# Optimization experiments

Measured on AMD Instinct MI355X. Metric: run time of the kernel, lower is better.

Reference implementation:

```python
import jax, jax.numpy as jnp
import numpy as np

B, C, H, W = 4, 288, 64, 64
P = 2
HEADS = 36
MLP_RATIO = 4.0
D = C * P * P              # hidden_size = 1152
HF = int(D * MLP_RATIO)    # 4608
LN_EPS = 1e-6
ATTN_EPS = 1e-8


def _layernorm(x):
    # LayerNorm over [C,H,W] per sample, no affine
    mu = jnp.mean(x, axis=(1, 2, 3), keepdims=True)
    var = jnp.mean((x - mu) ** 2, axis=(1, 2, 3), keepdims=True)
    return (x - mu) * jax.lax.rsqrt(var + LN_EPS)


def _seg(x):
    # b c (n1 p) (n2 p) -> b (n1 n2) (c p p)
    b, c, h, w = x.shape
    n1, n2 = h // P, w // P
    x = x.reshape(b, c, n1, P, n2, P).transpose(0, 2, 4, 1, 3, 5)
    return x.reshape(b, n1 * n2, c * P * P)


def _comb(t, h, w):
    # b (n1 n2) (c p p) -> b c (n1 p) (n2 p)
    b, n, dd = t.shape
    n1, n2 = h // P, w // P
    c = dd // (P * P)
    x = t.reshape(b, n1, n2, c, P, P).transpose(0, 3, 1, 4, 2, 5)
    return x.reshape(b, c, h, w)


def _lite_la(t, qkv_w, proj_w, proj_b):
    # ReLU-kernel linear attention with ones-padding normalization trick
    b, s, dm = t.shape
    d = dm // HEADS
    qkv = t @ qkv_w.T                       # [b,s,3*dm]
    q, k, v = jnp.split(qkv, 3, axis=-1)
    q = jax.nn.relu(q).reshape(b, s, HEADS, d)
    k = jax.nn.relu(k).reshape(b, s, HEADS, d)
    v = v.reshape(b, s, HEADS, d)
    v = jnp.concatenate([v, jnp.ones((b, s, HEADS, 1), v.dtype)], axis=-1)  # PAD_VAL=1
    vk = jnp.einsum('bshe,bshd->bhed', v, k)       # [b,h,d+1,d]
    out = jnp.einsum('bhed,bshd->bshe', vk, q)     # [b,s,h,d+1]
    out = out[..., :-1] / (out[..., -1:] + ATTN_EPS)
    return out.reshape(b, s, dm) @ proj_w.T + proj_b


def _glumb(t, inv_w, inv_b, dw_w, dw_b, pw_w):
    # GLU MBConv: 1x1 expand + SiLU -> 3x3 depthwise -> GLU gate -> 1x1 project
    b, n, c = t.shape
    hp = wp = int(n ** 0.5)
    x = t.reshape(b, hp, wp, c).transpose(0, 3, 1, 2)  # NCHW
    x = jnp.einsum('bchw,oc->bohw', x, inv_w[:, :, 0, 0]) + inv_b[None, :, None, None]
    x = jax.nn.silu(x)
    x = jax.lax.conv_general_dilated(x, dw_w, (1, 1), 'SAME',
                                     feature_group_count=dw_w.shape[0],
                                     dimension_numbers=('NCHW', 'OIHW', 'NCHW'))
    x = x + dw_b[None, :, None, None]
    x, gate = jnp.split(x, 2, axis=1)
    x = x * jax.nn.silu(gate)
    x = jnp.einsum('bchw,oc->bohw', x, pw_w[:, :, 0, 0])
    return x.reshape(b, c, n).transpose(0, 2, 1)


def setup_inputs() -> dict:
    key = jax.random.key(0)
    ks = jax.random.split(key, 10)
    s = 0.02
    return {
        'x': jax.random.normal(ks[0], (B, C, H, W), jnp.float32),
        'cond': jax.random.normal(ks[1], (B, 6 * C, H, W), jnp.float32),
        'global_token': jax.random.normal(ks[2], (B, D), jnp.float32),
        'time_token': jax.random.normal(ks[3], (B, D), jnp.float32),
        'ss_w': jax.random.normal(ks[4], (6 * C, 6 * C, 1, 1), jnp.float32) * s,
        'ss_b': jnp.zeros((6 * C,), jnp.float32),
        'qkv_w': jax.random.normal(ks[5], (3 * D, D), jnp.float32) * s,
        'proj_w': jax.random.normal(ks[6], (D, D), jnp.float32) * s,
        'proj_b': jnp.zeros((D,), jnp.float32),
        'inv_w': jax.random.normal(ks[7], (2 * HF, D, 1, 1), jnp.float32) * s,
        'inv_b': jnp.zeros((2 * HF,), jnp.float32),
        'dw_w': jax.random.normal(ks[8], (2 * HF, 1, 3, 3), jnp.float32) * s,
        'dw_b': jnp.zeros((2 * HF,), jnp.float32),
        'pw_w': jax.random.normal(ks[9], (D, HF, 1, 1), jnp.float32) * s,
    }


def reference(x, cond, global_token, time_token, ss_w, ss_b, qkv_w, proj_w, proj_b,
              inv_w, inv_b, dw_w, dw_b, pw_w):
    # scale_shift_table: SiLU + 1x1 conv on cond, chunk into 6 per-channel maps
    ss = jnp.einsum('bchw,oc->bohw', jax.nn.silu(cond), ss_w[:, :, 0, 0]) + ss_b[None, :, None, None]
    sh_msa, sc_msa, g_msa, sh_mlp, sc_mlp, g_mlp = jnp.split(ss, 6, axis=1)
    # attention branch
    tok = _seg(_layernorm(x) * (1.0 + sc_msa) + sh_msa)
    tok = jnp.concatenate([global_token[:, None], time_token[:, None], tok], axis=1)
    a = _lite_la(tok, qkv_w, proj_w, proj_b)
    x = x + _comb(a[:, 2:], H, W) * g_msa
    # MLP branch
    m = _glumb(_seg(_layernorm(x) * (1.0 + sc_mlp) + sh_mlp), inv_w, inv_b, dw_w, dw_b, pw_w)
    x = x + _comb(m, H, W) * g_mlp
    return x
```

## Files before the change

kernel.cpp:

```cpp
#include <hip/hip_runtime.h>
#include <hip/hip_bf16.h>
#include <cstdint>


typedef __bf16 bf16;
typedef bf16 bf16x8 __attribute__((ext_vector_type(8)));
typedef bf16 bf16x4 __attribute__((ext_vector_type(4)));
typedef float f32x4 __attribute__((ext_vector_type(4)));

typedef const __attribute__((address_space(1))) void gas_void;
typedef __attribute__((address_space(3))) void las_void;

__device__ __forceinline__ void gload16(const bf16* g, bf16* l) {
    __builtin_amdgcn_global_load_lds((gas_void*)g, (las_void*)l, 16, 0, 0);
}

#define BB 4
#define CC 288
#define HW 4096
#define C6 1728
#define DD 1152
#define SEQ 1026
#define RTOT 4104
#define NTOK 1024
#define HF 4608
#define HF2 9216
#define NPB 1179648

static constexpr size_t OFF_SUMS = 0;
static constexpr size_t OFF_SS   = 256;
static constexpr size_t SS_BYTES = (size_t)C6 * 16384 * 2;
static constexpr size_t OFF_R2   = OFF_SS + SS_BYTES;
static constexpr size_t OFF_PART1= OFF_R2;
static constexpr size_t OFF_A1   = OFF_R2;
static constexpr size_t OFF_T    = OFF_R2;
static constexpr size_t OFF_QKV  = OFF_T   + (size_t)RTOT*DD*2;
static constexpr size_t OFF_PART2= OFF_QKV;
static constexpr size_t OFF_VK   = OFF_QKV + (size_t)3456*RTOT*2;
static constexpr size_t OFF_ATT  = OFF_VK  + (size_t)144*1056*4;
static constexpr size_t OFF_APROJ= OFF_ATT + (size_t)RTOT*DD*2;
static constexpr size_t OFF_T2   = OFF_R2;
static constexpr size_t OFF_Y    = OFF_T2  + (size_t)4096*DD*2;
static constexpr size_t OFF_G    = OFF_Y   + (size_t)4096*HF2*2;
static constexpr size_t OFF_M    = OFF_G   + (size_t)4096*HF*2;
static constexpr size_t OFF_W    = OFF_R2  + 132120576;
static constexpr size_t OFF_WSS  = OFF_W;
static constexpr size_t OFF_WQKV = OFF_WSS  + (size_t)C6*C6*2;
static constexpr size_t OFF_WPROJ= OFF_WQKV + (size_t)3456*DD*2;
static constexpr size_t OFF_WINV = OFF_WPROJ+ (size_t)DD*DD*2;
static constexpr size_t OFF_WPW  = OFF_WINV + (size_t)HF2*DD*2;

__global__ __launch_bounds__(256) void cvt_bf16(const float* __restrict__ s,
                                                bf16* __restrict__ d, int n4) {
    int i = blockIdx.x * 256 + threadIdx.x;
    if (i < n4) {
        float4 v = ((const float4*)s)[i];
        bf16x4 o = {(bf16)v.x, (bf16)v.y, (bf16)v.z, (bf16)v.w};
        ((bf16x4*)d)[i] = o;
    }
}

__device__ __forceinline__ void block_reduce2_store(float s1, float s2, float* dst) {
    #pragma unroll
    for (int o = 32; o > 0; o >>= 1) { s1 += __shfl_down(s1, o); s2 += __shfl_down(s2, o); }
    __shared__ float r1[4], r2[4];
    int wave = threadIdx.x >> 6, lane = threadIdx.x & 63;
    if (lane == 0) { r1[wave] = s1; r2[wave] = s2; }
    __syncthreads();
    if (threadIdx.x == 0) {
        dst[0] = r1[0] + r1[1] + r1[2] + r1[3];
        dst[1] = r2[0] + r2[1] + r2[2] + r2[3];
    }
}

__global__ __launch_bounds__(256) void ln_stats(const float* __restrict__ x, float* __restrict__ part) {
    const float* base = x + (size_t)blockIdx.x * 4096;
    float s1 = 0.f, s2 = 0.f;
    #pragma unroll
    for (int it = 0; it < 4; it++) {
        float4 v = ((const float4*)base)[it * 256 + threadIdx.x];
        s1 += v.x + v.y + v.z + v.w;
        s2 += v.x * v.x + v.y * v.y + v.z * v.z + v.w * v.w;
    }
    block_reduce2_store(s1, s2, part + (size_t)blockIdx.x * 2);
}

__global__ __launch_bounds__(256) void reduce_part(const float* __restrict__ part, float* __restrict__ sums,
                                                   int nper, int out_off) {
    int b = blockIdx.x;
    float s1 = 0.f, s2 = 0.f;
    for (int i = threadIdx.x; i < nper; i += 256) {
        s1 += part[(size_t)(b * nper + i) * 2];
        s2 += part[(size_t)(b * nper + i) * 2 + 1];
    }
    block_reduce2_store(s1, s2, sums + out_off + b * 2);
}

__global__ __launch_bounds__(256) void prep_cond(const float* __restrict__ cond, bf16* __restrict__ A1) {
    __shared__ float tile[64][65];
    int b = blockIdx.z, k0 = blockIdx.y * 64, h0 = blockIdx.x * 64;
    int col = threadIdx.x & 63, r4 = threadIdx.x >> 6;
    const float* src = cond + ((size_t)b * C6 + k0) * HW + h0;
    #pragma unroll
    for (int p = 0; p < 16; p++) {
        int kk = r4 + p * 4;
        float v = src[(size_t)kk * HW + col];
        tile[col][kk] = v / (1.f + __expf(-v));
    }
    __syncthreads();
    bf16* dst = A1 + ((size_t)(b * HW + h0)) * C6 + k0;
    #pragma unroll
    for (int p = 0; p < 16; p++) {
        int rr = r4 + p * 4;
        dst[(size_t)rr * C6 + col] = (bf16)tile[rr][col];
    }
}

template <int EP, int BIAS>
__global__ __launch_bounds__(256) void gemm_bt(const bf16* __restrict__ A, const bf16* __restrict__ B,
                                               const float* __restrict__ bias, bf16* __restrict__ C,
                                               int M, int N, int K, int reluLimit) {
    __shared__ __align__(16) bf16 As[128 * 32];
    __shared__ __align__(16) bf16 Bs[128 * 32];
    const int tid = threadIdx.x, wave = tid >> 6, lane = tid & 63;
    const int m0 = blockIdx.y * 128, n0 = blockIdx.x * 128;

    const int c0 = wave * 128 + lane;
    const int c1 = c0 + 64;
    const int sw = ((c0 >> 2) & 3) ^ ((c0 >> 4) & 3);
    const int ka = (((c0 & 3) ^ sw)) * 8;
    int ra0 = min(m0 + (c0 >> 2), M - 1), ra1 = min(m0 + (c1 >> 2), M - 1);
    int rb0 = min(n0 + (c0 >> 2), N - 1), rb1 = min(n0 + (c1 >> 2), N - 1);
    const bf16* gA0 = A + (size_t)ra0 * K + ka;
    const bf16* gA1 = A + (size_t)ra1 * K + ka;
    const bf16* gB0 = B + (size_t)rb0 * K + ka;
    const bf16* gB1 = B + (size_t)rb1 * K + ka;
    bf16* lA0 = As + wave * 1024;
    bf16* lA1 = As + wave * 1024 + 512;
    bf16* lB0 = Bs + wave * 1024;
    bf16* lB1 = Bs + wave * 1024 + 512;

    const int wm = (wave >> 1) * 64, wn = (wave & 1) * 64;
    const int l15 = lane & 15;
    const int sr = (l15 & 3) ^ ((l15 >> 2) & 3);
    const int fc = ((lane >> 4) ^ sr) * 8;
    const bf16* fa = As + (wm + l15) * 32 + fc;
    const bf16* fb = Bs + (wn + l15) * 32 + fc;

    f32x4 acc[4][4];
    #pragma unroll
    for (int i = 0; i < 4; i++)
        #pragma unroll
        for (int j = 0; j < 4; j++) acc[i][j] = (f32x4){0.f, 0.f, 0.f, 0.f};

    for (int kt = 0; kt < K; kt += 32) {
        __syncthreads();
        gload16(gA0, lA0); gload16(gA1, lA1);
        gload16(gB0, lB0); gload16(gB1, lB1);
        gA0 += 32; gA1 += 32; gB0 += 32; gB1 += 32;
        __syncthreads();
        bf16x8 af[4], bv[4];
        #pragma unroll
        for (int i = 0; i < 4; i++) af[i] = *(const bf16x8*)(fa + i * 16 * 32);
        #pragma unroll
        for (int j = 0; j < 4; j++) bv[j] = *(const bf16x8*)(fb + j * 16 * 32);
        #pragma unroll
        for (int i = 0; i < 4; i++)
            #pragma unroll
            for (int j = 0; j < 4; j++)
                acc[i][j] = __builtin_amdgcn_mfma_f32_16x16x32_bf16(af[i], bv[j], acc[i][j], 0, 0, 0);
    }

    const int mq = (lane >> 4) * 4, nl = lane & 15;
    #pragma unroll
    for (int i = 0; i < 4; i++) {
        #pragma unroll
        for (int j = 0; j < 4; j++) {
            int n = n0 + wn + j * 16 + nl;
            if (n < N) {
                #pragma unroll
                for (int r = 0; r < 4; r++) {
                    int m = m0 + wm + i * 16 + mq + r;
                    if (m < M) {
                        float v = acc[i][j][r];
                        if (BIAS == 1) v += bias[m];
                        else if (BIAS == 2) v += bias[n];
                        if (EP == 1) { if (m < reluLimit) v = fmaxf(v, 0.f); }
                        else if (EP == 2) { v = v / (1.f + __expf(-v)); }
                        C[(size_t)m * N + n] = (bf16)v;
                    }
                }
            }
        }
    }
}

__global__ __launch_bounds__(256) void build_tok(const float* __restrict__ x, const float* __restrict__ gtok,
                                                 const float* __restrict__ ttok, const bf16* __restrict__ ss,
                                                 const float* __restrict__ sums, bf16* __restrict__ T) {
    int row = blockIdx.x;
    int b = row / SEQ, s = row % SEQ;
    bf16* dst = T + (size_t)row * DD;
    if (s == 0) {
        for (int d = threadIdx.x; d < DD; d += 256) dst[d] = (bf16)gtok[b * DD + d];
        return;
    }
    if (s == 1) {
        for (int d = threadIdx.x; d < DD; d += 256) dst[d] = (bf16)ttok[b * DD + d];
        return;
    }
    float mu = sums[b * 2] * (1.f / (float)NPB);
    float var = sums[b * 2 + 1] * (1.f / (float)NPB) - mu * mu;
    float rsig = rsqrtf(var + 1e-6f);
    int n = s - 2, n1 = n >> 5, n2 = n & 31;
    for (int dd = threadIdx.x; dd < DD; dd += 256) {
        int c = dd >> 2, p1 = (dd >> 1) & 1, p2 = dd & 1;
        int hw = (n1 * 2 + p1) * 64 + n2 * 2 + p2;
        float xv = x[((size_t)b * CC + c) * HW + hw];
        float sc = (float)ss[(size_t)(288 + c) * 16384 + b * HW + hw];
        float sh = (float)ss[(size_t)(0 + c) * 16384 + b * HW + hw];
        dst[dd] = (bf16)((xv - mu) * rsig * (1.f + sc) + sh);
    }
}

__global__ __launch_bounds__(256) void attn_vk(const bf16* __restrict__ qkv, float* __restrict__ vk) {
    int bh = blockIdx.x >> 2, sb = blockIdx.x & 3;
    int b = bh / 36, h = bh % 36;
    int s_begin = sb * 288;
    int s_end = min(s_begin + 288, SEQ);
    const bf16* kbase = qkv + (size_t)(DD + h * 32) * RTOT + b * SEQ;
    const bf16* vbase = qkv + (size_t)(2 * DD + h * 32) * RTOT + b * SEQ;
    __shared__ __align__(16) bf16 kk[32][80];
    __shared__ __align__(16) bf16 vv[32][80];
    int tid = threadIdx.x;
    int e = tid >> 3, dg = (tid & 7) * 4;
    int lrow = tid >> 3, lcol = (tid & 7) * 8;
    float a0 = 0.f, a1 = 0.f, a2 = 0.f, a3 = 0.f, aD = 0.f;
    for (int s0 = s_begin; s0 < s_end; s0 += 64) {
        __syncthreads();
        #pragma unroll
        for (int j = 0; j < 8; j++) {
            int s = s0 + lcol + j;
            bool ok = s < s_end;
            kk[lrow][lcol + j] = ok ? kbase[(size_t)lrow * RTOT + s] : (bf16)0.f;
            vv[lrow][lcol + j] = ok ? vbase[(size_t)lrow * RTOT + s] : (bf16)0.f;
        }
        __syncthreads();
        #pragma unroll
        for (int j0 = 0; j0 < 64; j0 += 8) {
            bf16x8 vvv = *(const bf16x8*)&vv[e][j0];
            bf16x8 k0 = *(const bf16x8*)&kk[dg + 0][j0];
            bf16x8 k1 = *(const bf16x8*)&kk[dg + 1][j0];
            bf16x8 k2 = *(const bf16x8*)&kk[dg + 2][j0];
            bf16x8 k3 = *(const bf16x8*)&kk[dg + 3][j0];
            #pragma unroll
            for (int j = 0; j < 8; j++) {
                float vf = (float)vvv[j];
                a0 += vf * (float)k0[j];
                a1 += vf * (float)k1[j];
                a2 += vf * (float)k2[j];
                a3 += vf * (float)k3[j];
            }
            if (tid < 32) {
                bf16x8 kd = *(const bf16x8*)&kk[tid][j0];
                #pragma unroll
                for (int j = 0; j < 8; j++) aD += (float)kd[j];
            }
        }
    }
    float* dst = vk + (size_t)bh * 1056;
    atomicAdd(&dst[e * 32 + dg + 0], a0);
    atomicAdd(&dst[e * 32 + dg + 1], a1);
    atomicAdd(&dst[e * 32 + dg + 2], a2);
    atomicAdd(&dst[e * 32 + dg + 3], a3);
    if (tid < 32) atomicAdd(&dst[1024 + tid], aD);
}

__global__ __launch_bounds__(256) void attn_out(const bf16* __restrict__ qkv, const float* __restrict__ vk,
                                                bf16* __restrict__ att) {
    int bh = blockIdx.y, b = bh / 36, h = bh % 36;
    int s0 = blockIdx.x * 64;
    __shared__ float vks[1056];
    __shared__ __align__(16) bf16 qs[32][80];
    int tid = threadIdx.x;
    for (int i = tid; i < 1056; i += 256) vks[i] = vk[(size_t)bh * 1056 + i];
    const bf16* qbase = qkv + (size_t)(h * 32) * RTOT + b * SEQ;
    int lrow = tid >> 3, lcol = (tid & 7) * 8;
    #pragma unroll
    for (int j = 0; j < 8; j++) {
        int s = s0 + lcol + j;
        qs[lrow][lcol + j] = (s < SEQ) ? qbase[(size_t)lrow * RTOT + s] : (bf16)0.f;
    }
    __syncthreads();
    int sl = tid >> 2, eg = (tid & 3) * 8;
    int s = s0 + sl;
    float num[8] = {0.f, 0.f, 0.f, 0.f, 0.f, 0.f, 0.f, 0.f};
    float den = 0.f;
    #pragma unroll
    for (int d = 0; d < 32; d++) {
        float qv = (float)qs[d][sl];
        den += vks[1024 + d] * qv;
        #pragma unroll
        for (int t = 0; t < 8; t++) num[t] += vks[(eg + t) * 32 + d] * qv;
    }
    if (s < SEQ) {
        float inv = 1.f / (den + 1e-8f);
        bf16* dst = att + ((size_t)(b * SEQ + s)) * DD + h * 32 + eg;
        #pragma unroll
        for (int t = 0; t < 8; t++) dst[t] = (bf16)(num[t] * inv);
    }
}

__global__ __launch_bounds__(256) void add_attn(const float* __restrict__ x, const bf16* __restrict__ aproj,
                                                const bf16* __restrict__ ss, float* __restrict__ xo,
                                                float* __restrict__ part) {
    int b = blockIdx.x / 4608;
    size_t idx = (size_t)blockIdx.x * 256 + threadIdx.x;
    size_t local = idx - (size_t)b * NPB;
    int c = (int)(local >> 12), hw = (int)(local & 4095);
    int hh = hw >> 6, w = hw & 63;
    int n = (hh >> 1) * 32 + (w >> 1);
    int dd = c * 4 + (hh & 1) * 2 + (w & 1);
    float a = (float)aproj[(size_t)dd * RTOT + b * SEQ + 2 + n];
    float g = (float)ss[(size_t)(576 + c) * 16384 + b * HW + hw];
    float v = x[idx] + a * g;
    xo[idx] = v;
    block_reduce2_store(v, v * v, part + (size_t)blockIdx.x * 2);
}

__global__ __launch_bounds__(256) void build_tok2(const float* __restrict__ x1, const bf16* __restrict__ ss,
                                                  const float* __restrict__ sums, bf16* __restrict__ T2) {
    int row = blockIdx.x, b = row >> 10, n = row & 1023;
    float mu = sums[8 + b * 2] * (1.f / (float)NPB);
    float var = sums[9 + b * 2] * (1.f / (float)NPB) - mu * mu;
    float rsig = rsqrtf(var + 1e-6f);
    int n1 = n >> 5, n2 = n & 31;
    bf16* dst = T2 + (size_t)row * DD;
    for (int dd = threadIdx.x; dd < DD; dd += 256) {
        int c = dd >> 2, p1 = (dd >> 1) & 1, p2 = dd & 1;
        int hw = (n1 * 2 + p1) * 64 + n2 * 2 + p2;
        float xv = x1[((size_t)b * CC + c) * HW + hw];
        float sc = (float)ss[(size_t)(1152 + c) * 16384 + b * HW + hw];
        float sh = (float)ss[(size_t)(864 + c) * 16384 + b * HW + hw];
        dst[dd] = (bf16)((xv - mu) * rsig * (1.f + sc) + sh);
    }
}

__global__ __launch_bounds__(256) void dwglu(const bf16* __restrict__ y, const float* __restrict__ dw_w,
                                             const float* __restrict__ dw_b, bf16* __restrict__ g) {
    __shared__ __align__(16) bf16 xs[6400];
    __shared__ __align__(16) bf16 gs[6400];
    int b = blockIdx.z, tile = blockIdx.y, c0 = blockIdx.x * 64;
    int ty = (tile >> 2) * 8, tx = (tile & 3) * 8;
    int tid = threadIdx.x, cc = tid & 63, pg = tid >> 6;
    for (int p = pg; p < 100; p += 4) {
        int py = ty + p / 10 - 1, px = tx + p % 10 - 1;
        bool in = (py >= 0 && py < 32 && px >= 0 && px < 32);
        size_t base = ((size_t)(b * NTOK + py * 32 + px)) * HF2;
        xs[p * 64 + cc] = in ? y[base + c0 + cc] : (bf16)0.f;
        gs[p * 64 + cc] = in ? y[base + HF + c0 + cc] : (bf16)0.f;
    }
    float wx[9], wg[9];
    #pragma unroll
    for (int t = 0; t < 9; t++) {
        wx[t] = dw_w[(size_t)(c0 + cc) * 9 + t];
        wg[t] = dw_w[(size_t)(HF + c0 + cc) * 9 + t];
    }
    float bx = dw_b[c0 + cc], bg = dw_b[HF + c0 + cc];
    __syncthreads();
    for (int p = pg * 16; p < pg * 16 + 16; p++) {
        int py = p >> 3, px = p & 7;
        float ax = bx, ag = bg;
        #pragma unroll
        for (int dy = 0; dy < 3; dy++)
            #pragma unroll
            for (int dx = 0; dx < 3; dx++) {
                int q = (py + dy) * 10 + (px + dx);
                ax += (float)xs[q * 64 + cc] * wx[dy * 3 + dx];
                ag += (float)gs[q * 64 + cc] * wg[dy * 3 + dx];
            }
        float out = ax * (ag / (1.f + __expf(-ag)));
        g[((size_t)(b * NTOK + (ty + py) * 32 + tx + px)) * HF + c0 + cc] = (bf16)out;
    }
}

__global__ __launch_bounds__(256) void add_mlp(const bf16* __restrict__ mm, const bf16* __restrict__ ss,
                                               float* __restrict__ xo) {
    int b = blockIdx.x / 4608;
    size_t idx = (size_t)blockIdx.x * 256 + threadIdx.x;
    size_t local = idx - (size_t)b * NPB;
    int c = (int)(local >> 12), hw = (int)(local & 4095);
    int hh = hw >> 6, w = hw & 63;
    int n = (hh >> 1) * 32 + (w >> 1);
    int dd = c * 4 + (hh & 1) * 2 + (w & 1);
    float mv = (float)mm[(size_t)dd * 4096 + b * NTOK + n];
    float g = (float)ss[(size_t)(1440 + c) * 16384 + b * HW + hw];
    xo[idx] = xo[idx] + mv * g;
}

extern "C" void kernel_launch(void* const* d_in, const int* in_sizes, int n_in,
                              void* d_out, int out_size, void* d_ws, size_t ws_size,
                              hipStream_t stream) {
    (void)in_sizes; (void)n_in; (void)out_size; (void)ws_size;
    const float* x      = (const float*)d_in[0];
    const float* cond   = (const float*)d_in[1];
    const float* gtok   = (const float*)d_in[2];
    const float* ttok   = (const float*)d_in[3];
    const float* ss_w   = (const float*)d_in[4];
    const float* ss_b   = (const float*)d_in[5];
    const float* qkv_w  = (const float*)d_in[6];
    const float* proj_w = (const float*)d_in[7];
    const float* proj_b = (const float*)d_in[8];
    const float* inv_w  = (const float*)d_in[9];
    const float* inv_b  = (const float*)d_in[10];
    const float* dw_w   = (const float*)d_in[11];
    const float* dw_b   = (const float*)d_in[12];
    const float* pw_w   = (const float*)d_in[13];
    float* out = (float*)d_out;
    char* ws = (char*)d_ws;

    float* sums  = (float*)(ws + OFF_SUMS);
    float* PART1 = (float*)(ws + OFF_PART1);
    float* PART2 = (float*)(ws + OFF_PART2);
    bf16* SS    = (bf16*)(ws + OFF_SS);
    bf16* A1    = (bf16*)(ws + OFF_A1);
    bf16* T     = (bf16*)(ws + OFF_T);
    bf16* QKV   = (bf16*)(ws + OFF_QKV);
    float* VK   = (float*)(ws + OFF_VK);
    bf16* ATT   = (bf16*)(ws + OFF_ATT);
    bf16* APROJ = (bf16*)(ws + OFF_APROJ);
    bf16* T2    = (bf16*)(ws + OFF_T2);
    bf16* Y     = (bf16*)(ws + OFF_Y);
    bf16* G     = (bf16*)(ws + OFF_G);
    bf16* MM    = (bf16*)(ws + OFF_M);
    bf16* WSS   = (bf16*)(ws + OFF_WSS);
    bf16* WQKV  = (bf16*)(ws + OFF_WQKV);
    bf16* WPROJ = (bf16*)(ws + OFF_WPROJ);
    bf16* WINV  = (bf16*)(ws + OFF_WINV);
    bf16* WPW   = (bf16*)(ws + OFF_WPW);

    cvt_bf16<<<2916, 256, 0, stream>>>(ss_w, WSS, C6 * C6 / 4);
    cvt_bf16<<<3888, 256, 0, stream>>>(qkv_w, WQKV, 3456 * DD / 4);
    cvt_bf16<<<1296, 256, 0, stream>>>(proj_w, WPROJ, DD * DD / 4);
    cvt_bf16<<<10368, 256, 0, stream>>>(inv_w, WINV, HF2 * DD / 4);
    cvt_bf16<<<5184, 256, 0, stream>>>(pw_w, WPW, DD * HF / 4);

    ln_stats<<<1152, 256, 0, stream>>>(x, PART1);
    reduce_part<<<4, 256, 0, stream>>>(PART1, sums, 288, 0);
    prep_cond<<<dim3(64, 27, 4), 256, 0, stream>>>(cond, A1);
    gemm_bt<0, 1><<<dim3(128, 14), 256, 0, stream>>>(WSS, A1, ss_b, SS, C6, 16384, C6, 0);
    build_tok<<<RTOT, 256, 0, stream>>>(x, gtok, ttok, SS, sums, T);
    gemm_bt<1, 0><<<dim3(33, 27), 256, 0, stream>>>(WQKV, T, nullptr, QKV, 3456, RTOT, DD, 2304);
    hipMemsetAsync(ws + OFF_VK, 0, (size_t)144 * 1056 * 4, stream);
    attn_vk<<<576, 256, 0, stream>>>(QKV, VK);
    attn_out<<<dim3(17, 144), 256, 0, stream>>>(QKV, VK, ATT);
    gemm_bt<0, 1><<<dim3(33, 9), 256, 0, stream>>>(WPROJ, ATT, proj_b, APROJ, DD, RTOT, DD, 0);
    add_attn<<<18432, 256, 0, stream>>>(x, APROJ, SS, out, PART2);
    reduce_part<<<4, 256, 0, stream>>>(PART2, sums, 4608, 8);
    build_tok2<<<4096, 256, 0, stream>>>(out, SS, sums, T2);
    gemm_bt<2, 2><<<dim3(72, 32), 256, 0, stream>>>(T2, WINV, inv_b, Y, 4096, HF2, DD, 0);
    dwglu<<<dim3(72, 16, 4), 256, 0, stream>>>(Y, dw_w, dw_b, G);
    gemm_bt<0, 0><<<dim3(32, 9), 256, 0, stream>>>(WPW, G, nullptr, MM, DD, 4096, HF, 0);
    add_mlp<<<18432, 256, 0, stream>>>(MM, SS, out);
}
```

Before: 1.138 ms.

## Tile token builders through shared memory and group GEMM block order

Replaces the per-row token builders, which made strided scattered reads from NCHW x and the scale/shift maps, with a tiled kernel. It reads 32 channels by two image rows with vectorized loads, transposes through shared memory, and writes 16-byte token rows. Global and time tokens move to a small separate copy kernel. The GEMM also remaps block indices into groups of 8 M-tiles so neighbouring blocks share A and B tiles in L2.

```diff
diff --git a/kernel.cpp b/kernel.cpp
--- a/kernel.cpp
+++ b/kernel.cpp
@@ -123,7 +123,14 @@
     __shared__ __align__(16) bf16 As[128 * 32];
     __shared__ __align__(16) bf16 Bs[128 * 32];
     const int tid = threadIdx.x, wave = tid >> 6, lane = tid & 63;
-    const int m0 = blockIdx.y * 128, n0 = blockIdx.x * 128;
+
+    const int nx = gridDim.x, ny = gridDim.y, G = 8;
+    int idx = blockIdx.y * nx + blockIdx.x;
+    int band = idx / (G * nx);
+    int r = idx - band * (G * nx);
+    int gm = min(G, ny - band * G);
+    const int m0 = (band * G + r % gm) * 128;
+    const int n0 = (r / gm) * 128;
 
     const int c0 = wave * 128 + lane;
     const int c1 = c0 + 64;
@@ -179,10 +186,10 @@
             int n = n0 + wn + j * 16 + nl;
             if (n < N) {
                 #pragma unroll
-                for (int r = 0; r < 4; r++) {
-                    int m = m0 + wm + i * 16 + mq + r;
+                for (int r2 = 0; r2 < 4; r2++) {
+                    int m = m0 + wm + i * 16 + mq + r2;
                     if (m < M) {
-                        float v = acc[i][j][r];
+                        float v = acc[i][j][r2];
                         if (BIAS == 1) v += bias[m];
                         else if (BIAS == 2) v += bias[n];
                         if (EP == 1) { if (m < reluLimit) v = fmaxf(v, 0.f); }
@@ -195,32 +202,48 @@
     }
 }
 
-__global__ __launch_bounds__(256) void build_tok(const float* __restrict__ x, const float* __restrict__ gtok,
-                                                 const float* __restrict__ ttok, const bf16* __restrict__ ss,
-                                                 const float* __restrict__ sums, bf16* __restrict__ T) {
-    int row = blockIdx.x;
-    int b = row / SEQ, s = row % SEQ;
-    bf16* dst = T + (size_t)row * DD;
-    if (s == 0) {
-        for (int d = threadIdx.x; d < DD; d += 256) dst[d] = (bf16)gtok[b * DD + d];
-        return;
-    }
-    if (s == 1) {
-        for (int d = threadIdx.x; d < DD; d += 256) dst[d] = (bf16)ttok[b * DD + d];
-        return;
-    }
-    float mu = sums[b * 2] * (1.f / (float)NPB);
-    float var = sums[b * 2 + 1] * (1.f / (float)NPB) - mu * mu;
+__global__ __launch_bounds__(256) void build_tok_t(const float* __restrict__ xs, const bf16* __restrict__ ss,
+                                                   const float* __restrict__ sums, int soff, int shb, int scb,
+                                                   bf16* __restrict__ dst, int tokoff, int seqstride) {
+    __shared__ bf16 tl[32][132];
+    int cch = blockIdx.x, n1 = blockIdx.y, b = blockIdx.z;
+    int c0 = cch * 32;
+    int tid = threadIdx.x, cl = tid >> 3, wseg = tid & 7;
+
+    float mu = sums[soff + b * 2] * (1.f / (float)NPB);
+    float var = sums[soff + b * 2 + 1] * (1.f / (float)NPB) - mu * mu;
     float rsig = rsqrtf(var + 1e-6f);
-    int n = s - 2, n1 = n >> 5, n2 = n & 31;
-    for (int dd = threadIdx.x; dd < DD; dd += 256) {
-        int c = dd >> 2, p1 = (dd >> 1) & 1, p2 = dd & 1;
-        int hw = (n1 * 2 + p1) * 64 + n2 * 2 + p2;
-        float xv = x[((size_t)b * CC + c) * HW + hw];
-        float sc = (float)ss[(size_t)(288 + c) * 16384 + b * HW + hw];
-        float sh = (float)ss[(size_t)(0 + c) * 16384 + b * HW + hw];
-        dst[dd] = (bf16)((xv - mu) * rsig * (1.f + sc) + sh);
-    }
+
+    int c = c0 + cl;
+    #pragma unroll
+    for (int hh = 0; hh < 2; hh++) {
+        int hw = (2 * n1 + hh) * 64 + wseg * 8;
+        const float* xp = xs + ((size_t)b * CC + c) * HW + hw;
+        float4 x0 = ((const float4*)xp)[0];
+        float4 x1 = ((const float4*)xp)[1];
+        bf16x8 scv = *(const bf16x8*)(ss + (size_t)(scb + c) * 16384 + b * HW + hw);
+        bf16x8 shv = *(const bf16x8*)(ss + (size_t)(shb + c) * 16384 + b * HW + hw);
+        float xv[8] = {x0.x, x0.y, x0.z, x0.w, x1.x, x1.y, x1.z, x1.w};
+        #pragma unroll
+        for (int k = 0; k < 8; k++) {
+            int w = wseg * 8 + k;
+            float v = (xv[k] - mu) * rsig * (1.f + (float)scv[k]) + (float)shv[k];
+            tl[w >> 1][cl * 4 + hh * 2 + (w & 1)] = (bf16)v;
+        }
+    }
+    __syncthreads();
+    int token = tid >> 3, seg = (tid & 7) * 16;
+    bf16* drow = dst + ((size_t)(b * seqstride + tokoff + n1 * 32 + token)) * DD + c0 * 4 + seg;
+    *(bf16x8*)drow = *(const bf16x8*)&tl[token][seg];
+    *(bf16x8*)(drow + 8) = *(const bf16x8*)&tl[token][seg + 8];
+}
+
+__global__ __launch_bounds__(256) void copy_gt(const float* __restrict__ gtok, const float* __restrict__ ttok,
+                                               bf16* __restrict__ T) {
+    int which = blockIdx.x, b = blockIdx.y;
+    const float* src = (which == 0 ? gtok : ttok) + b * DD;
+    bf16* dst = T + (size_t)(b * SEQ + which) * DD;
+    for (int d = threadIdx.x; d < DD; d += 256) dst[d] = (bf16)src[d];
 }
 
 __global__ __launch_bounds__(256) void attn_vk(const bf16* __restrict__ qkv, float* __restrict__ vk) {
@@ -328,24 +351,6 @@
     block_reduce2_store(v, v * v, part + (size_t)blockIdx.x * 2);
 }
 
-__global__ __launch_bounds__(256) void build_tok2(const float* __restrict__ x1, const bf16* __restrict__ ss,
-                                                  const float* __restrict__ sums, bf16* __restrict__ T2) {
-    int row = blockIdx.x, b = row >> 10, n = row & 1023;
-    float mu = sums[8 + b * 2] * (1.f / (float)NPB);
-    float var = sums[9 + b * 2] * (1.f / (float)NPB) - mu * mu;
-    float rsig = rsqrtf(var + 1e-6f);
-    int n1 = n >> 5, n2 = n & 31;
-    bf16* dst = T2 + (size_t)row * DD;
-    for (int dd = threadIdx.x; dd < DD; dd += 256) {
-        int c = dd >> 2, p1 = (dd >> 1) & 1, p2 = dd & 1;
-        int hw = (n1 * 2 + p1) * 64 + n2 * 2 + p2;
-        float xv = x1[((size_t)b * CC + c) * HW + hw];
-        float sc = (float)ss[(size_t)(1152 + c) * 16384 + b * HW + hw];
-        float sh = (float)ss[(size_t)(864 + c) * 16384 + b * HW + hw];
-        dst[dd] = (bf16)((xv - mu) * rsig * (1.f + sc) + sh);
-    }
-}
-
 __global__ __launch_bounds__(256) void dwglu(const bf16* __restrict__ y, const float* __restrict__ dw_w,
                                              const float* __restrict__ dw_b, bf16* __restrict__ g) {
     __shared__ __align__(16) bf16 xs[6400];
@@ -449,7 +454,8 @@
     reduce_part<<<4, 256, 0, stream>>>(PART1, sums, 288, 0);
     prep_cond<<<dim3(64, 27, 4), 256, 0, stream>>>(cond, A1);
     gemm_bt<0, 1><<<dim3(128, 14), 256, 0, stream>>>(WSS, A1, ss_b, SS, C6, 16384, C6, 0);
-    build_tok<<<RTOT, 256, 0, stream>>>(x, gtok, ttok, SS, sums, T);
+    build_tok_t<<<dim3(9, 32, 4), 256, 0, stream>>>(x, SS, sums, 0, 0, 288, T, 2, SEQ);
+    copy_gt<<<dim3(2, 4), 256, 0, stream>>>(gtok, ttok, T);
     gemm_bt<1, 0><<<dim3(33, 27), 256, 0, stream>>>(WQKV, T, nullptr, QKV, 3456, RTOT, DD, 2304);
     hipMemsetAsync(ws + OFF_VK, 0, (size_t)144 * 1056 * 4, stream);
     attn_vk<<<576, 256, 0, stream>>>(QKV, VK);
@@ -457,7 +463,7 @@
     gemm_bt<0, 1><<<dim3(33, 9), 256, 0, stream>>>(WPROJ, ATT, proj_b, APROJ, DD, RTOT, DD, 0);
     add_attn<<<18432, 256, 0, stream>>>(x, APROJ, SS, out, PART2);
     reduce_part<<<4, 256, 0, stream>>>(PART2, sums, 4608, 8);
-    build_tok2<<<4096, 256, 0, stream>>>(out, SS, sums, T2);
+    build_tok_t<<<dim3(9, 32, 4), 256, 0, stream>>>(out, SS, sums, 8, 864, 1152, T2, 0, 1024);
     gemm_bt<2, 2><<<dim3(72, 32), 256, 0, stream>>>(T2, WINV, inv_b, Y, 4096, HF2, DD, 0);
     dwglu<<<dim3(72, 16, 4), 256, 0, stream>>>(Y, dw_w, dw_b, G);
     gemm_bt<0, 0><<<dim3(32, 9), 256, 0, stream>>>(WPW, G, nullptr, MM, DD, 4096, HF, 0);
```

Measured after the change: 1.074 ms. 5.6% less time.
